# Optimization experiments

Measured on AMD Instinct MI355X. Metric: run time of the kernel, lower is better.

Reference implementation:

```python
import jax, jax.numpy as jnp
import numpy as np

TOP_K = 2

def setup_inputs() -> dict:
    key = jax.random.key(0)
    k1, k2, k3, k4, k5 = jax.random.split(key, 5)
    T, H, I, E = 2048, 2048, 2048, 8
    scale = 0.02
    return {
        "hidden_states": jax.random.normal(k1, (T, H), dtype=jnp.float32),
        "gate_w": jax.random.normal(k2, (E, H), dtype=jnp.float32) * scale,  # router Linear weight [E, H]
        "w1": jax.random.normal(k3, (E, H, I), dtype=jnp.float32) * scale,   # gate proj per expert
        "w3": jax.random.normal(k4, (E, H, I), dtype=jnp.float32) * scale,   # up proj per expert
        "w2": jax.random.normal(k5, (E, I, H), dtype=jnp.float32) * scale,   # down proj per expert
    }

def reference(hidden_states, gate_w, w1, w3, w2):
    T, H = hidden_states.shape
    E = gate_w.shape[0]
    # Router gate in float32 (ReplicatedLinear with params_dtype=float32, no bias)
    router_logits = jnp.einsum('th,eh->te', hidden_states.astype(jnp.float32), gate_w)
    probs = jax.nn.softmax(router_logits, axis=-1)  # [T, E]
    topk_w, topk_idx = jax.lax.top_k(probs, TOP_K)   # [T, K]
    topk_w = topk_w / jnp.sum(topk_w, axis=-1, keepdims=True)  # renormalize=True
    # Dense combine weights: zero for non-selected experts
    rows = jnp.arange(T)[:, None]
    comb = jnp.zeros((T, E), dtype=hidden_states.dtype).at[rows, topk_idx].add(
        topk_w.astype(hidden_states.dtype))
    # SwiGLU experts computed densely per expert, masked-combined
    g = jnp.einsum('th,ehi->tei', hidden_states, w1)   # gate proj
    u = jnp.einsum('th,ehi->tei', hidden_states, w3)   # up proj
    act = jax.nn.silu(g) * u                            # [T, E, I]
    y = jnp.einsum('tei,eih->teh', act, w2)             # down proj [T, E, H]
    out = jnp.einsum('te,teh->th', comb, y)             # weighted combine
    return out
```

## Files before the change

kernel.cpp:

```cpp
#include <hip/hip_runtime.h>
#include <hip/hip_bf16.h>

#define T_TOK 2048
#define H_DIM 2048
#define I_DIM 2048
#define E_NUM 8
#define TOPK  2

#define BM 128
#define BN 64
#define BK 64

typedef float  floatx4 __attribute__((ext_vector_type(4)));
typedef __bf16 bf16x8  __attribute__((ext_vector_type(8)));
typedef __bf16 bf16x4  __attribute__((ext_vector_type(4)));

__device__ __forceinline__ int swz(int row, int g) {
    return (row * 8 + (g ^ ((row >> 1) & 7))) * 16;
}

__global__ __launch_bounds__(64) void router_kernel(
    const float* __restrict__ hs, const float* __restrict__ gate_w,
    int* __restrict__ counts, int* __restrict__ lists, float* __restrict__ wpair,
    __bf16* __restrict__ Xbf)
{
    const int t    = blockIdx.x;
    const int lane = threadIdx.x;

    float acc[E_NUM];
#pragma unroll
    for (int e = 0; e < E_NUM; e++) acc[e] = 0.f;

    const float4* hsrow = (const float4*)(hs + (size_t)t * H_DIM);
#pragma unroll
    for (int it = 0; it < (H_DIM / 4) / 64; it++) {
        const int c = lane + it * 64;
        const float4 x = hsrow[c];
        const bf16x4 v = {(__bf16)x.x, (__bf16)x.y, (__bf16)x.z, (__bf16)x.w};
        *(bf16x4*)(Xbf + (size_t)t * H_DIM + 4 * c) = v;
#pragma unroll
        for (int e = 0; e < E_NUM; e++) {
            const float4 w = ((const float4*)(gate_w + (size_t)e * H_DIM))[c];
            acc[e] += x.x * w.x + x.y * w.y + x.z * w.z + x.w * w.w;
        }
    }
#pragma unroll
    for (int e = 0; e < E_NUM; e++) {
        float v = acc[e];
        for (int off = 32; off >= 1; off >>= 1) v += __shfl_xor(v, off, 64);
        acc[e] = v;
    }
    if (lane == 0) {
        float l0 = -1e30f; int i0 = 0;
        for (int e = 0; e < E_NUM; e++) if (acc[e] > l0) { l0 = acc[e]; i0 = e; }
        float l1 = -1e30f; int i1 = (i0 == 0) ? 1 : 0;
        for (int e = 0; e < E_NUM; e++) if (e != i0 && acc[e] > l1) { l1 = acc[e]; i1 = e; }
        const float e1 = __expf(l1 - l0);
        const float s  = 1.f + e1;
        const int p0 = atomicAdd(&counts[i0], 1);
        lists[i0 * T_TOK + p0] = 2 * t;
        const int p1 = atomicAdd(&counts[i1], 1);
        lists[i1 * T_TOK + p1] = 2 * t + 1;
        wpair[2 * t]     = 1.f / s;
        wpair[2 * t + 1] = e1 / s;
    }
}

__global__ __launch_bounds__(256, 3) void gemm1_kernel(
    const __bf16* __restrict__ Xbf, const float* __restrict__ w1,
    const float* __restrict__ w3, const int* __restrict__ counts,
    const int* __restrict__ lists, __bf16* __restrict__ Abuf)
{
    const int e   = blockIdx.z;
    const int n_e = counts[e];
    const int m0  = blockIdx.y * BM;
    if (m0 >= n_e) return;
    const int n0 = blockIdx.x * BN;

    const int*   list = lists + e * T_TOK;
    const float* w1e  = w1 + (size_t)e * H_DIM * I_DIM;
    const float* w3e  = w3 + (size_t)e * H_DIM * I_DIM;

    __shared__ __align__(16) __bf16 Xs [BM * BK];
    __shared__ __align__(16) __bf16 B1s[BN * BK];
    __shared__ __align__(16) __bf16 B3s[BN * BK];

    const int tid = threadIdx.x;
    const int xr8 = tid >> 3;
    const int xg  = tid & 7;
    const int kb = tid >> 5;
    const int np = tid & 31;

    int tok[4];
#pragma unroll
    for (int i = 0; i < 4; i++) {
        const int r = m0 + xr8 + 32 * i;
        tok[i] = (r < n_e) ? (list[r] >> 1) : 0;
    }

    const int wave = tid >> 6;
    const int lane = tid & 63;
    const int wm   = (wave >> 1) * 64;
    const int wn   = (wave & 1) * 32;
    const int lrow = lane & 15;
    const int quad = lane >> 4;

    floatx4 accG[4][2], accU[4][2];
#pragma unroll
    for (int i = 0; i < 4; i++)
#pragma unroll
        for (int j = 0; j < 2; j++) {
            accG[i][j] = (floatx4){0.f, 0.f, 0.f, 0.f};
            accU[i][j] = (floatx4){0.f, 0.f, 0.f, 0.f};
        }

    for (int k0 = 0; k0 < H_DIM; k0 += BK) {
#pragma unroll
        for (int i = 0; i < 4; i++) {
            const int m = xr8 + 32 * i;
            const bf16x8 v = *(const bf16x8*)(Xbf + (size_t)tok[i] * H_DIM + k0 + 8 * xg);
            *(bf16x8*)((char*)Xs + swz(m, xg)) = v;
        }
        {
            const float* src = w1e + (size_t)(k0 + 8 * kb) * I_DIM + n0 + 2 * np;
            float2 f[8];
#pragma unroll
            for (int j = 0; j < 8; j++) f[j] = *(const float2*)(src + (size_t)j * I_DIM);
            bf16x8 wlo, whi;
#pragma unroll
            for (int j = 0; j < 8; j++) { wlo[j] = (__bf16)f[j].x; whi[j] = (__bf16)f[j].y; }
            *(bf16x8*)((char*)B1s + swz(2 * np,     kb)) = wlo;
            *(bf16x8*)((char*)B1s + swz(2 * np + 1, kb)) = whi;
        }
        {
            const float* src = w3e + (size_t)(k0 + 8 * kb) * I_DIM + n0 + 2 * np;
            float2 f[8];
#pragma unroll
            for (int j = 0; j < 8; j++) f[j] = *(const float2*)(src + (size_t)j * I_DIM);
            bf16x8 wlo, whi;
#pragma unroll
            for (int j = 0; j < 8; j++) { wlo[j] = (__bf16)f[j].x; whi[j] = (__bf16)f[j].y; }
            *(bf16x8*)((char*)B3s + swz(2 * np,     kb)) = wlo;
            *(bf16x8*)((char*)B3s + swz(2 * np + 1, kb)) = whi;
        }
        __syncthreads();

#pragma unroll
        for (int s = 0; s < 2; s++) {
            bf16x8 af[4], b1f[2], b3f[2];
#pragma unroll
            for (int i = 0; i < 4; i++)
                af[i]  = *(const bf16x8*)((char*)Xs  + swz(wm + i * 16 + lrow, 4 * s + quad));
#pragma unroll
            for (int j = 0; j < 2; j++) {
                b1f[j] = *(const bf16x8*)((char*)B1s + swz(wn + j * 16 + lrow, 4 * s + quad));
                b3f[j] = *(const bf16x8*)((char*)B3s + swz(wn + j * 16 + lrow, 4 * s + quad));
            }
#pragma unroll
            for (int i = 0; i < 4; i++)
#pragma unroll
                for (int j = 0; j < 2; j++) {
                    accG[i][j] = __builtin_amdgcn_mfma_f32_16x16x32_bf16(af[i], b1f[j], accG[i][j], 0, 0, 0);
                    accU[i][j] = __builtin_amdgcn_mfma_f32_16x16x32_bf16(af[i], b3f[j], accU[i][j], 0, 0, 0);
                }
        }
        __syncthreads();
    }

#pragma unroll
    for (int i = 0; i < 4; i++) {
#pragma unroll
        for (int r = 0; r < 4; r++) {
            const int row = m0 + wm + i * 16 + quad * 4 + r;
            if (row < n_e) {
                const int p = list[row];
                __bf16* dst = Abuf + (size_t)p * I_DIM + n0 + wn + lrow;
#pragma unroll
                for (int j = 0; j < 2; j++) {
                    const float g = accG[i][j][r];
                    const float u = accU[i][j][r];
                    const float sv = g / (1.f + __expf(-g));
                    dst[j * 16] = (__bf16)(sv * u);
                }
            }
        }
    }
}

__global__ __launch_bounds__(256, 4) void gemm2_kernel(
    const __bf16* __restrict__ Abuf, const float* __restrict__ w2,
    const int* __restrict__ counts, const int* __restrict__ lists,
    __bf16* __restrict__ Ybuf)
{
    const int e   = blockIdx.z;
    const int n_e = counts[e];
    const int m0  = blockIdx.y * BM;
    if (m0 >= n_e) return;
    const int n0 = blockIdx.x * BN;

    const int*   list = lists + e * T_TOK;
    const float* w2e  = w2 + (size_t)e * I_DIM * H_DIM;

    __shared__ __align__(16) __bf16 As[BM * BK];
    __shared__ __align__(16) __bf16 Bs[BN * BK];

    const int tid = threadIdx.x;
    const int ar8 = tid >> 3;
    const int ag  = tid & 7;
    const int kb  = tid >> 5;
    const int np  = tid & 31;

    int prow[4];
#pragma unroll
    for (int i = 0; i < 4; i++) {
        const int r = m0 + ar8 + 32 * i;
        prow[i] = (r < n_e) ? list[r] : 0;
    }

    const int wave = tid >> 6;
    const int lane = tid & 63;
    const int wm   = (wave >> 1) * 64;
    const int wn   = (wave & 1) * 32;
    const int lrow = lane & 15;
    const int quad = lane >> 4;

    floatx4 acc[4][2];
#pragma unroll
    for (int i = 0; i < 4; i++)
#pragma unroll
        for (int j = 0; j < 2; j++) acc[i][j] = (floatx4){0.f, 0.f, 0.f, 0.f};

    for (int k0 = 0; k0 < I_DIM; k0 += BK) {
#pragma unroll
        for (int i = 0; i < 4; i++) {
            const int m = ar8 + 32 * i;
            const bf16x8 v = *(const bf16x8*)(Abuf + (size_t)prow[i] * I_DIM + k0 + 8 * ag);
            *(bf16x8*)((char*)As + swz(m, ag)) = v;
        }
        {
            const float* src = w2e + (size_t)(k0 + 8 * kb) * H_DIM + n0 + 2 * np;
            float2 f[8];
#pragma unroll
            for (int j = 0; j < 8; j++) f[j] = *(const float2*)(src + (size_t)j * H_DIM);
            bf16x8 wlo, whi;
#pragma unroll
            for (int j = 0; j < 8; j++) { wlo[j] = (__bf16)f[j].x; whi[j] = (__bf16)f[j].y; }
            *(bf16x8*)((char*)Bs + swz(2 * np,     kb)) = wlo;
            *(bf16x8*)((char*)Bs + swz(2 * np + 1, kb)) = whi;
        }
        __syncthreads();

#pragma unroll
        for (int s = 0; s < 2; s++) {
            bf16x8 af[4], bf[2];
#pragma unroll
            for (int i = 0; i < 4; i++)
                af[i] = *(const bf16x8*)((char*)As + swz(wm + i * 16 + lrow, 4 * s + quad));
#pragma unroll
            for (int j = 0; j < 2; j++)
                bf[j] = *(const bf16x8*)((char*)Bs + swz(wn + j * 16 + lrow, 4 * s + quad));
#pragma unroll
            for (int i = 0; i < 4; i++)
#pragma unroll
                for (int j = 0; j < 2; j++)
                    acc[i][j] = __builtin_amdgcn_mfma_f32_16x16x32_bf16(af[i], bf[j], acc[i][j], 0, 0, 0);
        }
        __syncthreads();
    }

#pragma unroll
    for (int i = 0; i < 4; i++) {
#pragma unroll
        for (int r = 0; r < 4; r++) {
            const int row = m0 + wm + i * 16 + quad * 4 + r;
            if (row < n_e) {
                const int p = list[row];
                __bf16* dst = Ybuf + (size_t)p * H_DIM + n0 + wn + lrow;
#pragma unroll
                for (int j = 0; j < 2; j++) dst[j * 16] = (__bf16)acc[i][j][r];
            }
        }
    }
}

__global__ __launch_bounds__(256) void combine_kernel(
    const __bf16* __restrict__ Ybuf, const float* __restrict__ wpair,
    float* __restrict__ out)
{
    const int idx = blockIdx.x * 256 + threadIdx.x;
    const int t   = idx >> 9;
    const int hc  = (idx & 511) * 4;
    const float w0 = wpair[2 * t];
    const float w1 = wpair[2 * t + 1];
    const __bf16* y0 = Ybuf + (size_t)(2 * t) * H_DIM + hc;
    const __bf16* y1 = y0 + H_DIM;
    float4 o;
    o.x = w0 * (float)y0[0] + w1 * (float)y1[0];
    o.y = w0 * (float)y0[1] + w1 * (float)y1[1];
    o.z = w0 * (float)y0[2] + w1 * (float)y1[2];
    o.w = w0 * (float)y0[3] + w1 * (float)y1[3];
    *(float4*)(out + (size_t)t * H_DIM + hc) = o;
}

extern "C" void kernel_launch(void* const* d_in, const int* in_sizes, int n_in,
                              void* d_out, int out_size, void* d_ws, size_t ws_size,
                              hipStream_t stream)
{
    const float* hs     = (const float*)d_in[0];
    const float* gate_w = (const float*)d_in[1];
    const float* w1     = (const float*)d_in[2];
    const float* w3     = (const float*)d_in[3];
    const float* w2     = (const float*)d_in[4];
    float*       out    = (float*)d_out;

    char* ws = (char*)d_ws;
    int*    counts = (int*)(ws + 0);
    float*  wpair  = (float*)(ws + 1024);
    int*    lists  = (int*)(ws + 32768);
    __bf16* Xbf    = (__bf16*)(ws + (1 << 17));
    __bf16* Ybuf   = (__bf16*)(ws + (1 << 17));
    __bf16* Abuf   = (__bf16*)(ws + (1 << 17) +
                               (size_t)2 * T_TOK * H_DIM * sizeof(__bf16));

    hipMemsetAsync(counts, 0, E_NUM * sizeof(int), stream);

    router_kernel<<<T_TOK, 64, 0, stream>>>(hs, gate_w, counts, lists, wpair, Xbf);

    gemm1_kernel<<<dim3(I_DIM / BN, T_TOK / BM, E_NUM), 256, 0, stream>>>(
        Xbf, w1, w3, counts, lists, Abuf);

    gemm2_kernel<<<dim3(H_DIM / BN, T_TOK / BM, E_NUM), 256, 0, stream>>>(
        Abuf, w2, counts, lists, Ybuf);

    combine_kernel<<<(T_TOK * H_DIM / 4) / 256, 256, 0, stream>>>(Ybuf, wpair, out);
}
```

Measured before the change: 598.0 us.

## Pre-convert expert weights to transposed bf16 and load tiles via global_load_lds

Adds a kernel that converts w1/w3/w2 to bf16 in a K-contiguous transposed layout into workspace. The GEMMs then stream bf16 tiles directly into LDS with global_load_lds instead of loading fp32, converting and storing through registers. gemm2 widens its N tile to 128, the router packs 4 tokens per block, and combine uses vector loads. This costs an extra full pass over all weights each call and needs a large workspace, with the old path kept as a fallback.

```diff
diff --git a/kernel.cpp b/kernel.cpp
--- a/kernel.cpp
+++ b/kernel.cpp
@@ -5,11 +5,6 @@
 #define H_DIM 2048
 #define I_DIM 2048
 #define E_NUM 8
-#define TOPK  2
-
-#define BM 128
-#define BN 64
-#define BK 64
 
 typedef float  floatx4 __attribute__((ext_vector_type(4)));
 typedef __bf16 bf16x8  __attribute__((ext_vector_type(8)));
@@ -19,13 +14,19 @@
     return (row * 8 + (g ^ ((row >> 1) & 7))) * 16;
 }
 
-__global__ __launch_bounds__(64) void router_kernel(
+typedef const __attribute__((address_space(1))) void* as1_cptr;
+typedef __attribute__((address_space(3))) void*       as3_ptr;
+__device__ __forceinline__ void glds16(const void* g, void* l) {
+    __builtin_amdgcn_global_load_lds((as1_cptr)g, (as3_ptr)l, 16, 0, 0);
+}
+
+__global__ __launch_bounds__(256) void router_kernel(
     const float* __restrict__ hs, const float* __restrict__ gate_w,
     int* __restrict__ counts, int* __restrict__ lists, float* __restrict__ wpair,
     __bf16* __restrict__ Xbf)
 {
-    const int t    = blockIdx.x;
-    const int lane = threadIdx.x;
+    const int t    = blockIdx.x * 4 + (threadIdx.x >> 6);
+    const int lane = threadIdx.x & 63;
 
     float acc[E_NUM];
 #pragma unroll
@@ -66,40 +67,71 @@
     }
 }
 
-__global__ __launch_bounds__(256, 3) void gemm1_kernel(
-    const __bf16* __restrict__ Xbf, const float* __restrict__ w1,
-    const float* __restrict__ w3, const int* __restrict__ counts,
+__global__ __launch_bounds__(256) void convert_kernel(
+    const float* __restrict__ w1, const float* __restrict__ w3,
+    const float* __restrict__ w2, __bf16* __restrict__ Wb)
+{
+    const int z  = blockIdx.z;
+    const int m  = z >> 3;
+    const int n0 = blockIdx.x * 64;
+    const int k0 = blockIdx.y * 64;
+    const float* src = (m == 0 ? w1 : (m == 1 ? w3 : w2))
+                     + (size_t)(z & 7) * H_DIM * I_DIM;
+    __bf16* dst = Wb + (size_t)z * H_DIM * I_DIM;
+
+    const int lane = threadIdx.x & 63;
+    const int wq   = threadIdx.x >> 6;
+    const int n  = n0 + lane;
+    const int kb = k0 + 16 * wq;
+
+    float v[16];
+#pragma unroll
+    for (int j = 0; j < 16; j++) v[j] = src[(size_t)(kb + j) * 2048 + n];
+    bf16x8 lo, hi;
+#pragma unroll
+    for (int j = 0; j < 8; j++) { lo[j] = (__bf16)v[j]; hi[j] = (__bf16)v[8 + j]; }
+    *(bf16x8*)(dst + (size_t)n * 2048 + kb)     = lo;
+    *(bf16x8*)(dst + (size_t)n * 2048 + kb + 8) = hi;
+}
+
+__global__ __launch_bounds__(256, 3) void gemm1_bf(
+    const __bf16* __restrict__ Xbf, const __bf16* __restrict__ W1b,
+    const __bf16* __restrict__ W3b, const int* __restrict__ counts,
     const int* __restrict__ lists, __bf16* __restrict__ Abuf)
 {
     const int e   = blockIdx.z;
     const int n_e = counts[e];
-    const int m0  = blockIdx.y * BM;
+    const int m0  = blockIdx.y * 128;
     if (m0 >= n_e) return;
-    const int n0 = blockIdx.x * BN;
-
-    const int*   list = lists + e * T_TOK;
-    const float* w1e  = w1 + (size_t)e * H_DIM * I_DIM;
-    const float* w3e  = w3 + (size_t)e * H_DIM * I_DIM;
-
-    __shared__ __align__(16) __bf16 Xs [BM * BK];
-    __shared__ __align__(16) __bf16 B1s[BN * BK];
-    __shared__ __align__(16) __bf16 B3s[BN * BK];
-
-    const int tid = threadIdx.x;
-    const int xr8 = tid >> 3;
-    const int xg  = tid & 7;
-    const int kb = tid >> 5;
-    const int np = tid & 31;
-
-    int tok[4];
-#pragma unroll
-    for (int i = 0; i < 4; i++) {
-        const int r = m0 + xr8 + 32 * i;
-        tok[i] = (r < n_e) ? (list[r] >> 1) : 0;
-    }
-
-    const int wave = tid >> 6;
-    const int lane = tid & 63;
+    const int n0 = blockIdx.x * 64;
+
+    const int*    list = lists + e * T_TOK;
+    const __bf16* w1e  = W1b + (size_t)e * H_DIM * I_DIM;
+    const __bf16* w3e  = W3b + (size_t)e * H_DIM * I_DIM;
+
+    __shared__ __align__(16) __bf16 Xs [128 * 64];
+    __shared__ __align__(16) __bf16 B1s[64 * 64];
+    __shared__ __align__(16) __bf16 B3s[64 * 64];
+
+    const int tid = threadIdx.x, wave = tid >> 6, lane = tid & 63;
+
+    size_t xoff[4];
+#pragma unroll
+    for (int i = 0; i < 4; i++) {
+        const int row = wave * 32 + i * 8 + (lane >> 3);
+        const int r   = m0 + row;
+        const int tok = (r < n_e) ? (list[r] >> 1) : 0;
+        const int g   = (lane & 7) ^ ((4 * i + (lane >> 4)) & 7);
+        xoff[i] = (size_t)tok * H_DIM + 8 * g;
+    }
+    size_t boff[2];
+#pragma unroll
+    for (int i = 0; i < 2; i++) {
+        const int row = wave * 16 + i * 8 + (lane >> 3);
+        const int g   = (lane & 7) ^ ((4 * i + (lane >> 4)) & 7);
+        boff[i] = (size_t)(n0 + row) * H_DIM + 8 * g;
+    }
+
     const int wm   = (wave >> 1) * 64;
     const int wn   = (wave & 1) * 32;
     const int lrow = lane & 15;
@@ -114,34 +146,14 @@
             accU[i][j] = (floatx4){0.f, 0.f, 0.f, 0.f};
         }
 
-    for (int k0 = 0; k0 < H_DIM; k0 += BK) {
-#pragma unroll
-        for (int i = 0; i < 4; i++) {
-            const int m = xr8 + 32 * i;
-            const bf16x8 v = *(const bf16x8*)(Xbf + (size_t)tok[i] * H_DIM + k0 + 8 * xg);
-            *(bf16x8*)((char*)Xs + swz(m, xg)) = v;
-        }
-        {
-            const float* src = w1e + (size_t)(k0 + 8 * kb) * I_DIM + n0 + 2 * np;
-            float2 f[8];
-#pragma unroll
-            for (int j = 0; j < 8; j++) f[j] = *(const float2*)(src + (size_t)j * I_DIM);
-            bf16x8 wlo, whi;
-#pragma unroll
-            for (int j = 0; j < 8; j++) { wlo[j] = (__bf16)f[j].x; whi[j] = (__bf16)f[j].y; }
-            *(bf16x8*)((char*)B1s + swz(2 * np,     kb)) = wlo;
-            *(bf16x8*)((char*)B1s + swz(2 * np + 1, kb)) = whi;
-        }
-        {
-            const float* src = w3e + (size_t)(k0 + 8 * kb) * I_DIM + n0 + 2 * np;
-            float2 f[8];
-#pragma unroll
-            for (int j = 0; j < 8; j++) f[j] = *(const float2*)(src + (size_t)j * I_DIM);
-            bf16x8 wlo, whi;
-#pragma unroll
-            for (int j = 0; j < 8; j++) { wlo[j] = (__bf16)f[j].x; whi[j] = (__bf16)f[j].y; }
-            *(bf16x8*)((char*)B3s + swz(2 * np,     kb)) = wlo;
-            *(bf16x8*)((char*)B3s + swz(2 * np + 1, kb)) = whi;
+    for (int k0 = 0; k0 < H_DIM; k0 += 64) {
+#pragma unroll
+        for (int i = 0; i < 4; i++)
+            glds16(Xbf + xoff[i] + k0, Xs + (wave * 4 + i) * 512);
+#pragma unroll
+        for (int i = 0; i < 2; i++) {
+            glds16(w1e + boff[i] + k0, B1s + (wave * 2 + i) * 512);
+            glds16(w3e + boff[i] + k0, B3s + (wave * 2 + i) * 512);
         }
         __syncthreads();
 
@@ -187,34 +199,118 @@
     }
 }
 
-__global__ __launch_bounds__(256, 4) void gemm2_kernel(
-    const __bf16* __restrict__ Abuf, const float* __restrict__ w2,
+__global__ __launch_bounds__(256, 3) void gemm2_bf(
+    const __bf16* __restrict__ Abuf, const __bf16* __restrict__ W2b,
     const int* __restrict__ counts, const int* __restrict__ lists,
     __bf16* __restrict__ Ybuf)
 {
     const int e   = blockIdx.z;
     const int n_e = counts[e];
-    const int m0  = blockIdx.y * BM;
+    const int m0  = blockIdx.y * 128;
     if (m0 >= n_e) return;
-    const int n0 = blockIdx.x * BN;
+    const int n0 = blockIdx.x * 128;
+
+    const int*    list = lists + e * T_TOK;
+    const __bf16* w2e  = W2b + (size_t)e * H_DIM * I_DIM;
+
+    __shared__ __align__(16) __bf16 As[128 * 64];
+    __shared__ __align__(16) __bf16 Bs[128 * 64];
+
+    const int tid = threadIdx.x, wave = tid >> 6, lane = tid & 63;
+
+    size_t aoff[4], boff[4];
+#pragma unroll
+    for (int i = 0; i < 4; i++) {
+        const int row = wave * 32 + i * 8 + (lane >> 3);
+        const int r   = m0 + row;
+        const int p   = (r < n_e) ? list[r] : 0;
+        const int g   = (lane & 7) ^ ((4 * i + (lane >> 4)) & 7);
+        aoff[i] = (size_t)p * I_DIM + 8 * g;
+        boff[i] = (size_t)(n0 + row) * I_DIM + 8 * g;
+    }
+
+    const int wm   = (wave >> 1) * 64;
+    const int wn   = (wave & 1) * 64;
+    const int lrow = lane & 15;
+    const int quad = lane >> 4;
+
+    floatx4 acc[4][4];
+#pragma unroll
+    for (int i = 0; i < 4; i++)
+#pragma unroll
+        for (int j = 0; j < 4; j++) acc[i][j] = (floatx4){0.f, 0.f, 0.f, 0.f};
+
+    for (int k0 = 0; k0 < I_DIM; k0 += 64) {
+#pragma unroll
+        for (int i = 0; i < 4; i++) {
+            glds16(Abuf + aoff[i] + k0, As + (wave * 4 + i) * 512);
+            glds16(w2e  + boff[i] + k0, Bs + (wave * 4 + i) * 512);
+        }
+        __syncthreads();
+
+#pragma unroll
+        for (int s = 0; s < 2; s++) {
+            bf16x8 af[4], bf[4];
+#pragma unroll
+            for (int i = 0; i < 4; i++)
+                af[i] = *(const bf16x8*)((char*)As + swz(wm + i * 16 + lrow, 4 * s + quad));
+#pragma unroll
+            for (int j = 0; j < 4; j++)
+                bf[j] = *(const bf16x8*)((char*)Bs + swz(wn + j * 16 + lrow, 4 * s + quad));
+#pragma unroll
+            for (int i = 0; i < 4; i++)
+#pragma unroll
+                for (int j = 0; j < 4; j++)
+                    acc[i][j] = __builtin_amdgcn_mfma_f32_16x16x32_bf16(af[i], bf[j], acc[i][j], 0, 0, 0);
+        }
+        __syncthreads();
+    }
+
+#pragma unroll
+    for (int i = 0; i < 4; i++) {
+#pragma unroll
+        for (int r = 0; r < 4; r++) {
+            const int row = m0 + wm + i * 16 + quad * 4 + r;
+            if (row < n_e) {
+                const int p = list[row];
+                __bf16* dst = Ybuf + (size_t)p * H_DIM + n0 + wn + lrow;
+#pragma unroll
+                for (int j = 0; j < 4; j++) dst[j * 16] = (__bf16)acc[i][j][r];
+            }
+        }
+    }
+}
+
+__global__ __launch_bounds__(256, 3) void gemm1_fb(
+    const __bf16* __restrict__ Xbf, const float* __restrict__ w1,
+    const float* __restrict__ w3, const int* __restrict__ counts,
+    const int* __restrict__ lists, __bf16* __restrict__ Abuf)
+{
+    const int e   = blockIdx.z;
+    const int n_e = counts[e];
+    const int m0  = blockIdx.y * 128;
+    if (m0 >= n_e) return;
+    const int n0 = blockIdx.x * 64;
 
     const int*   list = lists + e * T_TOK;
-    const float* w2e  = w2 + (size_t)e * I_DIM * H_DIM;
-
-    __shared__ __align__(16) __bf16 As[BM * BK];
-    __shared__ __align__(16) __bf16 Bs[BN * BK];
+    const float* w1e  = w1 + (size_t)e * H_DIM * I_DIM;
+    const float* w3e  = w3 + (size_t)e * H_DIM * I_DIM;
+
+    __shared__ __align__(16) __bf16 Xs [128 * 64];
+    __shared__ __align__(16) __bf16 B1s[64 * 64];
+    __shared__ __align__(16) __bf16 B3s[64 * 64];
 
     const int tid = threadIdx.x;
-    const int ar8 = tid >> 3;
-    const int ag  = tid & 7;
+    const int xr8 = tid >> 3;
+    const int xg  = tid & 7;
     const int kb  = tid >> 5;
     const int np  = tid & 31;
 
-    int prow[4];
-#pragma unroll
-    for (int i = 0; i < 4; i++) {
-        const int r = m0 + ar8 + 32 * i;
-        prow[i] = (r < n_e) ? list[r] : 0;
+    int tok[4];
+#pragma unroll
+    for (int i = 0; i < 4; i++) {
+        const int r = m0 + xr8 + 32 * i;
+        tok[i] = (r < n_e) ? (list[r] >> 1) : 0;
     }
 
     const int wave = tid >> 6;
@@ -224,13 +320,132 @@
     const int lrow = lane & 15;
     const int quad = lane >> 4;
 
+    floatx4 accG[4][2], accU[4][2];
+#pragma unroll
+    for (int i = 0; i < 4; i++)
+#pragma unroll
+        for (int j = 0; j < 2; j++) {
+            accG[i][j] = (floatx4){0.f, 0.f, 0.f, 0.f};
+            accU[i][j] = (floatx4){0.f, 0.f, 0.f, 0.f};
+        }
+
+    for (int k0 = 0; k0 < H_DIM; k0 += 64) {
+#pragma unroll
+        for (int i = 0; i < 4; i++) {
+            const int m = xr8 + 32 * i;
+            const bf16x8 v = *(const bf16x8*)(Xbf + (size_t)tok[i] * H_DIM + k0 + 8 * xg);
+            *(bf16x8*)((char*)Xs + swz(m, xg)) = v;
+        }
+        {
+            const float* src = w1e + (size_t)(k0 + 8 * kb) * I_DIM + n0 + 2 * np;
+            float2 f[8];
+#pragma unroll
+            for (int j = 0; j < 8; j++) f[j] = *(const float2*)(src + (size_t)j * I_DIM);
+            bf16x8 wlo, whi;
+#pragma unroll
+            for (int j = 0; j < 8; j++) { wlo[j] = (__bf16)f[j].x; whi[j] = (__bf16)f[j].y; }
+            *(bf16x8*)((char*)B1s + swz(2 * np,     kb)) = wlo;
+            *(bf16x8*)((char*)B1s + swz(2 * np + 1, kb)) = whi;
+        }
+        {
+            const float* src = w3e + (size_t)(k0 + 8 * kb) * I_DIM + n0 + 2 * np;
+            float2 f[8];
+#pragma unroll
+            for (int j = 0; j < 8; j++) f[j] = *(const float2*)(src + (size_t)j * I_DIM);
+            bf16x8 wlo, whi;
+#pragma unroll
+            for (int j = 0; j < 8; j++) { wlo[j] = (__bf16)f[j].x; whi[j] = (__bf16)f[j].y; }
+            *(bf16x8*)((char*)B3s + swz(2 * np,     kb)) = wlo;
+            *(bf16x8*)((char*)B3s + swz(2 * np + 1, kb)) = whi;
+        }
+        __syncthreads();
+
+#pragma unroll
+        for (int s = 0; s < 2; s++) {
+            bf16x8 af[4], b1f[2], b3f[2];
+#pragma unroll
+            for (int i = 0; i < 4; i++)
+                af[i]  = *(const bf16x8*)((char*)Xs  + swz(wm + i * 16 + lrow, 4 * s + quad));
+#pragma unroll
+            for (int j = 0; j < 2; j++) {
+                b1f[j] = *(const bf16x8*)((char*)B1s + swz(wn + j * 16 + lrow, 4 * s + quad));
+                b3f[j] = *(const bf16x8*)((char*)B3s + swz(wn + j * 16 + lrow, 4 * s + quad));
+            }
+#pragma unroll
+            for (int i = 0; i < 4; i++)
+#pragma unroll
+                for (int j = 0; j < 2; j++) {
+                    accG[i][j] = __builtin_amdgcn_mfma_f32_16x16x32_bf16(af[i], b1f[j], accG[i][j], 0, 0, 0);
+                    accU[i][j] = __builtin_amdgcn_mfma_f32_16x16x32_bf16(af[i], b3f[j], accU[i][j], 0, 0, 0);
+                }
+        }
+        __syncthreads();
+    }
+
+#pragma unroll
+    for (int i = 0; i < 4; i++) {
+#pragma unroll
+        for (int r = 0; r < 4; r++) {
+            const int row = m0 + wm + i * 16 + quad * 4 + r;
+            if (row < n_e) {
+                const int p = list[row];
+                __bf16* dst = Abuf + (size_t)p * I_DIM + n0 + wn + lrow;
+#pragma unroll
+                for (int j = 0; j < 2; j++) {
+                    const float g = accG[i][j][r];
+                    const float u = accU[i][j][r];
+                    const float sv = g / (1.f + __expf(-g));
+                    dst[j * 16] = (__bf16)(sv * u);
+                }
+            }
+        }
+    }
+}
+
+__global__ __launch_bounds__(256, 3) void gemm2_fb(
+    const __bf16* __restrict__ Abuf, const float* __restrict__ w2,
+    const int* __restrict__ counts, const int* __restrict__ lists,
+    __bf16* __restrict__ Ybuf)
+{
+    const int e   = blockIdx.z;
+    const int n_e = counts[e];
+    const int m0  = blockIdx.y * 128;
+    if (m0 >= n_e) return;
+    const int n0 = blockIdx.x * 64;
+
+    const int*   list = lists + e * T_TOK;
+    const float* w2e  = w2 + (size_t)e * I_DIM * H_DIM;
+
+    __shared__ __align__(16) __bf16 As[128 * 64];
+    __shared__ __align__(16) __bf16 Bs[64 * 64];
+
+    const int tid = threadIdx.x;
+    const int ar8 = tid >> 3;
+    const int ag  = tid & 7;
+    const int kb  = tid >> 5;
+    const int np  = tid & 31;
+
+    int prow[4];
+#pragma unroll
+    for (int i = 0; i < 4; i++) {
+        const int r = m0 + ar8 + 32 * i;
+        prow[i] = (r < n_e) ? list[r] : 0;
+    }
+
+    const int wave = tid >> 6;
+    const int lane = tid & 63;
+    const int wm   = (wave >> 1) * 64;
+    const int wn   = (wave & 1) * 32;
+    const int lrow = lane & 15;
+    const int quad = lane >> 4;
+
     floatx4 acc[4][2];
 #pragma unroll
     for (int i = 0; i < 4; i++)
 #pragma unroll
         for (int j = 0; j < 2; j++) acc[i][j] = (floatx4){0.f, 0.f, 0.f, 0.f};
 
-    for (int k0 = 0; k0 < I_DIM; k0 += BK) {
+    for (int k0 = 0; k0 < I_DIM; k0 += 64) {
 #pragma unroll
         for (int i = 0; i < 4; i++) {
             const int m = ar8 + 32 * i;
@@ -294,11 +509,13 @@
     const float w1 = wpair[2 * t + 1];
     const __bf16* y0 = Ybuf + (size_t)(2 * t) * H_DIM + hc;
     const __bf16* y1 = y0 + H_DIM;
+    const bf16x4 a0 = *(const bf16x4*)y0;
+    const bf16x4 a1 = *(const bf16x4*)y1;
     float4 o;
-    o.x = w0 * (float)y0[0] + w1 * (float)y1[0];
-    o.y = w0 * (float)y0[1] + w1 * (float)y1[1];
-    o.z = w0 * (float)y0[2] + w1 * (float)y1[2];
-    o.w = w0 * (float)y0[3] + w1 * (float)y1[3];
+    o.x = w0 * (float)a0[0] + w1 * (float)a1[0];
+    o.y = w0 * (float)a0[1] + w1 * (float)a1[1];
+    o.z = w0 * (float)a0[2] + w1 * (float)a1[2];
+    o.w = w0 * (float)a0[3] + w1 * (float)a1[3];
     *(float4*)(out + (size_t)t * H_DIM + hc) = o;
 }
 
@@ -317,20 +534,43 @@
     int*    counts = (int*)(ws + 0);
     float*  wpair  = (float*)(ws + 1024);
     int*    lists  = (int*)(ws + 32768);
-    __bf16* Xbf    = (__bf16*)(ws + (1 << 17));
-    __bf16* Ybuf   = (__bf16*)(ws + (1 << 17));
-    __bf16* Abuf   = (__bf16*)(ws + (1 << 17) +
-                               (size_t)2 * T_TOK * H_DIM * sizeof(__bf16));
+
+    const size_t MAT  = (size_t)H_DIM * I_DIM;
+    const size_t WBB  = (size_t)3 * E_NUM * MAT * 2;
+    const size_t XB   = (size_t)T_TOK * H_DIM * 2;
+    const size_t AB   = (size_t)2 * T_TOK * I_DIM * 2;
+    const size_t YB   = (size_t)2 * T_TOK * H_DIM * 2;
+    const size_t BASE = (size_t)1 << 17;
+    const size_t need_big = BASE + WBB + XB + AB + YB;
 
     hipMemsetAsync(counts, 0, E_NUM * sizeof(int), stream);
 
-    router_kernel<<<T_TOK, 64, 0, stream>>>(hs, gate_w, counts, lists, wpair, Xbf);
-
-    gemm1_kernel<<<dim3(I_DIM / BN, T_TOK / BM, E_NUM), 256, 0, stream>>>(
-        Xbf, w1, w3, counts, lists, Abuf);
-
-    gemm2_kernel<<<dim3(H_DIM / BN, T_TOK / BM, E_NUM), 256, 0, stream>>>(
-        Abuf, w2, counts, lists, Ybuf);
-
-    combine_kernel<<<(T_TOK * H_DIM / 4) / 256, 256, 0, stream>>>(Ybuf, wpair, out);
-}
+    if (ws_size >= need_big) {
+        __bf16* Wb   = (__bf16*)(ws + BASE);
+        __bf16* Xbf  = (__bf16*)(ws + BASE + WBB);
+        __bf16* Abuf = (__bf16*)(ws + BASE + WBB + XB);
+        __bf16* Ybuf = (__bf16*)(ws + BASE + WBB + XB + AB);
+        __bf16* W1b  = Wb;
+        __bf16* W3b  = Wb + (size_t)E_NUM * MAT;
+        __bf16* W2b  = Wb + (size_t)2 * E_NUM * MAT;
+
+        convert_kernel<<<dim3(32, 32, 24), 256, 0, stream>>>(w1, w3, w2, Wb);
+        router_kernel<<<T_TOK / 4, 256, 0, stream>>>(hs, gate_w, counts, lists, wpair, Xbf);
+        gemm1_bf<<<dim3(I_DIM / 64, T_TOK / 128, E_NUM), 256, 0, stream>>>(
+            Xbf, W1b, W3b, counts, lists, Abuf);
+        gemm2_bf<<<dim3(H_DIM / 128, T_TOK / 128, E_NUM), 256, 0, stream>>>(
+            Abuf, W2b, counts, lists, Ybuf);
+        combine_kernel<<<(T_TOK * H_DIM / 4) / 256, 256, 0, stream>>>(Ybuf, wpair, out);
+    } else {
+        __bf16* Xbf  = (__bf16*)(ws + BASE);
+        __bf16* Ybuf = (__bf16*)(ws + BASE);
+        __bf16* Abuf = (__bf16*)(ws + BASE + YB);
+
+        router_kernel<<<T_TOK / 4, 256, 0, stream>>>(hs, gate_w, counts, lists, wpair, Xbf);
+        gemm1_fb<<<dim3(I_DIM / 64, T_TOK / 128, E_NUM), 256, 0, stream>>>(
+            Xbf, w1, w3, counts, lists, Abuf);
+        gemm2_fb<<<dim3(H_DIM / 64, T_TOK / 128, E_NUM), 256, 0, stream>>>(
+            Abuf, w2, counts, lists, Ybuf);
+        combine_kernel<<<(T_TOK * H_DIM / 4) / 256, 256, 0, stream>>>(Ybuf, wpair, out);
+    }
+}
```

Measured after the change: 647.0 us. 8.2% more time.
